# Kernel optimization log

Measured on AMD Instinct MI355X. Metric: run time of the kernel, lower is better.

## Reference

```python
import jax, jax.numpy as jnp
import numpy as np
import math

V = 32000      # vocab_size
D = 1024       # hidden_dims
T_MAX = 1024   # max_txt_len
L = 4          # n_layers
H = 8          # heads (fixed in CausalMHA)
HD = D // H
B, T = 2, 1024
EPS = 1e-5


def setup_inputs() -> dict:
    key = jax.random.key(0)
    ks = jax.random.split(key, 20)
    s = 0.02
    inp = {
        "x": jax.random.randint(ks[0], (B, T), 0, V, dtype=jnp.int64) if jax.config.read("jax_enable_x64") else jax.random.randint(ks[0], (B, T), 0, V, dtype=jnp.int32),
        "tok_emb": jax.random.normal(ks[1], (V, D), jnp.float32) * s,
        "pos_emb": jax.random.normal(ks[2], (1, T_MAX, D), jnp.float32) * s,
        "ln1_g": jnp.ones((L, D), jnp.float32),
        "ln1_b": jnp.zeros((L, D), jnp.float32),
        "wqkv": jax.random.normal(ks[3], (L, D, 3 * D), jnp.float32) * s,
        "bqkv": jnp.zeros((L, 3 * D), jnp.float32),
        "wo": jax.random.normal(ks[4], (L, D, D), jnp.float32) * s,
        "bo": jnp.zeros((L, D), jnp.float32),
        "ln2_g": jnp.ones((L, D), jnp.float32),
        "ln2_b": jnp.zeros((L, D), jnp.float32),
        "wfc": jax.random.normal(ks[5], (L, D, 4 * D), jnp.float32) * s,   # no bias
        "wfc2": jax.random.normal(ks[6], (L, 4 * D, D), jnp.float32) * s,  # no bias
        "fn_g": jnp.ones((D,), jnp.float32),
        "fn_b": jnp.zeros((D,), jnp.float32),
        "wout": jax.random.normal(ks[7], (D, V), jnp.float32) * s,
        "bout": jnp.zeros((V,), jnp.float32),
    }
    return inp


def _ln(x, g, b):
    mu = jnp.mean(x, axis=-1, keepdims=True)
    var = jnp.var(x, axis=-1, keepdims=True)
    return (x - mu) * jax.lax.rsqrt(var + EPS) * g + b


def _attn(xn, wqkv_l, bqkv_l, wo_l, bo_l):
    Bb, Tt, _ = xn.shape
    qkv = xn @ wqkv_l + bqkv_l                      # [B,T,3D]
    q, k, v = jnp.split(qkv, 3, axis=-1)
    q = q.reshape(Bb, Tt, H, HD)
    k = k.reshape(Bb, Tt, H, HD)
    v = v.reshape(Bb, Tt, H, HD)
    scores = jnp.einsum("bqhd,bkhd->bhqk", q, k) / math.sqrt(HD)
    mask = jnp.triu(jnp.ones((Tt, Tt), bool), k=1)   # True above diagonal
    scores = jnp.where(mask, jnp.float32(-jnp.inf), scores)
    att = jax.nn.softmax(scores, axis=-1)
    out = jnp.einsum("bhqk,bkhd->bqhd", att, v).reshape(Bb, Tt, D)
    return out @ wo_l + bo_l


def reference(x, tok_emb, pos_emb, ln1_g, ln1_b, wqkv, bqkv, wo, bo,
              ln2_g, ln2_b, wfc, wfc2, fn_g, fn_b, wout, bout):
    Tt = x.shape[1]
    h = tok_emb[x] + pos_emb[:, :Tt, :]              # [B,T,D]
    for i in range(L):
        h = h + _attn(_ln(h, ln1_g[i], ln1_b[i]), wqkv[i], bqkv[i], wo[i], bo[i])
        hn = _ln(h, ln2_g[i], ln2_b[i])
        h = h + jax.nn.gelu(hn @ wfc[i], approximate=False) @ wfc2[i]
    h = _ln(h, fn_g, fn_b)
    return h @ wout + bout                           # [B,T,V] logits
```

## Files before the change

### kernel.cpp

```cpp
#include <hip/hip_runtime.h>
#include <math.h>
#include <stdint.h>

#define D_  1024
#define T_  1024
#define H_  8
#define HD_ 128
#define L_  4
#define V_  32000
#define M_  2048

typedef __attribute__((ext_vector_type(4))) float f32x4;
typedef __attribute__((ext_vector_type(4))) short s16x4;
typedef __attribute__((ext_vector_type(8))) short s16x8;
typedef unsigned short u16;

__device__ __forceinline__ u16 f2bf(float f) {
  union { float f; uint32_t u; } c; c.f = f;
  uint32_t r = c.u + 0x7fffu + ((c.u >> 16) & 1u);
  return (u16)(r >> 16);
}
__device__ __forceinline__ float bf2f(u16 h) {
  union { uint32_t u; float f; } c; c.u = ((uint32_t)h) << 16;
  return c.f;
}
__device__ __forceinline__ float gelu_f(float x) {
  return 0.5f * x * (1.0f + erff(x * 0.70710678118654752f));
}

__device__ __forceinline__ void gload16(const u16* g, u16* l) {
  __builtin_amdgcn_global_load_lds(
      (const __attribute__((address_space(1))) void*)(uintptr_t)g,
      (__attribute__((address_space(3))) void*)(uint32_t)(uintptr_t)l,
      16, 0, 0);
}

__device__ __forceinline__ void convT_f32_tile(const float* __restrict__ in,
                                               u16* __restrict__ out,
                                               int ldin, int ldout,
                                               int c0, int r0,
                                               u16 (*tile)[72])
{
  const int t = threadIdx.x;
  const int rr = t >> 2, cs = (t & 3) << 4;
  u16 tmp[16];
  const float* p = in + (size_t)(r0 + rr) * ldin + c0 + cs;
#pragma unroll
  for (int q = 0; q < 4; ++q) {
    f32x4 v = *(const f32x4*)(p + q * 4);
#pragma unroll
    for (int j = 0; j < 4; ++j) tmp[q * 4 + j] = f2bf(v[j]);
  }
  *(s16x8*)&tile[rr][cs]     = *(const s16x8*)tmp;
  *(s16x8*)&tile[rr][cs + 8] = *(const s16x8*)(tmp + 8);
  __syncthreads();
  const int cr = t >> 2, rs = (t & 3) << 4;
  u16 o[16];
#pragma unroll
  for (int j = 0; j < 16; ++j) o[j] = tile[rs + j][cr];
  u16* op = out + (size_t)(c0 + cr) * ldout + r0 + rs;
  *(s16x8*)op       = *(const s16x8*)o;
  *(s16x8*)(op + 8) = *(const s16x8*)(o + 8);
}

__device__ __forceinline__
void ln_row_body(int row, float* __restrict__ hbuf, const float* __restrict__ P,
                 const float* __restrict__ g, const float* __restrict__ b,
                 u16* __restrict__ y, int red, float* red_s)
{
  const int tid = threadIdx.x;
  const size_t i = (size_t)row * D_ + tid * 4;
  f32x4 v = *(const f32x4*)&hbuf[i];
  if (red) {
#pragma unroll
    for (int zp = 0; zp < 4; ++zp) {
      f32x4 p = *(const f32x4*)&P[(size_t)zp * M_ * D_ + i];
      v[0] += p[0]; v[1] += p[1]; v[2] += p[2]; v[3] += p[3];
    }
    *(f32x4*)&hbuf[i] = v;
  }
  float s  = v[0] + v[1] + v[2] + v[3];
  float s2 = v[0]*v[0] + v[1]*v[1] + v[2]*v[2] + v[3]*v[3];
#pragma unroll
  for (int off = 32; off > 0; off >>= 1) {
    s  += __shfl_xor(s, off);
    s2 += __shfl_xor(s2, off);
  }
  if ((tid & 63) == 0) { red_s[tid >> 6] = s; red_s[4 + (tid >> 6)] = s2; }
  __syncthreads();
  s  = red_s[0] + red_s[1] + red_s[2] + red_s[3];
  s2 = red_s[4] + red_s[5] + red_s[6] + red_s[7];
  const float mean = s * (1.0f / D_);
  const float var  = s2 * (1.0f / D_) - mean * mean;
  const float rs   = rsqrtf(var + 1e-5f);
  f32x4 gg = *(const f32x4*)&g[tid * 4];
  f32x4 bb = *(const f32x4*)&b[tid * 4];
  u16 o[4];
#pragma unroll
  for (int j = 0; j < 4; ++j) o[j] = f2bf((v[j] - mean) * rs * gg[j] + bb[j]);
  *(s16x4*)&y[i] = *(const s16x4*)o;
}

__global__ __launch_bounds__(256)
void conv4ln_kernel(const float* __restrict__ wqkv_l, const float* __restrict__ wo_l,
                    const float* __restrict__ wfc_l, const float* __restrict__ wfc2_l,
                    u16* __restrict__ Wq, u16* __restrict__ Wo,
                    u16* __restrict__ Wf1, u16* __restrict__ Wf2,
                    float* __restrict__ hbuf, const float* __restrict__ P,
                    const float* __restrict__ g, const float* __restrict__ b,
                    u16* __restrict__ y, int red)
{
  __shared__ __align__(16) u16 tile[64][72];
  int f = blockIdx.x;
  if (f < 2048) { ln_row_body(f, hbuf, P, g, b, y, red, (float*)tile); return; }
  f -= 2048;
  if (f < 768) {
    convT_f32_tile(wqkv_l, Wq, 3 * D_, D_, (f % 48) << 6, (f / 48) << 6, tile);
  } else if (f < 1024) {
    f -= 768;
    convT_f32_tile(wo_l, Wo, D_, D_, (f & 15) << 6, (f >> 4) << 6, tile);
  } else if (f < 2048) {
    f -= 1024;
    convT_f32_tile(wfc_l, Wf1, 4 * D_, D_, (f & 63) << 6, (f >> 6) << 6, tile);
  } else {
    f -= 2048;
    convT_f32_tile(wfc2_l, Wf2, D_, 4 * D_, (f & 15) << 6, (f >> 4) << 6, tile);
  }
}

__global__ __launch_bounds__(256)
void convwout_ln(const float* __restrict__ wout, u16* __restrict__ WoutT,
                 float* __restrict__ hbuf, const float* __restrict__ P,
                 const float* __restrict__ g, const float* __restrict__ b,
                 u16* __restrict__ y)
{
  __shared__ __align__(16) u16 tile[64][72];
  int f = blockIdx.x;
  if (f < 2048) { ln_row_body(f, hbuf, P, g, b, y, 1, (float*)tile); return; }
  f -= 2048;
  convT_f32_tile(wout, WoutT, V_, D_, (f % 500) << 6, (f / 500) << 6, tile);
}

__global__ __launch_bounds__(256)
void ln_fold4(float* __restrict__ hbuf, const float* __restrict__ P,
              const float* __restrict__ bo, const float* __restrict__ g,
              const float* __restrict__ b, u16* __restrict__ y)
{
  __shared__ float red_s[8];
  const int row = blockIdx.x, tid = threadIdx.x;
  const size_t i = (size_t)row * D_ + tid * 4;
  f32x4 v = *(const f32x4*)&hbuf[i];
  f32x4 bb4 = *(const f32x4*)&bo[tid * 4];
#pragma unroll
  for (int zp = 0; zp < 4; ++zp) {
    f32x4 p = *(const f32x4*)&P[(size_t)zp * M_ * D_ + i];
    v[0] += p[0]; v[1] += p[1]; v[2] += p[2]; v[3] += p[3];
  }
#pragma unroll
  for (int j = 0; j < 4; ++j) v[j] += bb4[j];
  *(f32x4*)&hbuf[i] = v;
  float s  = v[0] + v[1] + v[2] + v[3];
  float s2 = v[0]*v[0] + v[1]*v[1] + v[2]*v[2] + v[3]*v[3];
#pragma unroll
  for (int off = 32; off > 0; off >>= 1) {
    s  += __shfl_xor(s, off);
    s2 += __shfl_xor(s2, off);
  }
  if ((tid & 63) == 0) { red_s[tid >> 6] = s; red_s[4 + (tid >> 6)] = s2; }
  __syncthreads();
  s  = red_s[0] + red_s[1] + red_s[2] + red_s[3];
  s2 = red_s[4] + red_s[5] + red_s[6] + red_s[7];
  const float mean = s * (1.0f / D_);
  const float var  = s2 * (1.0f / D_) - mean * mean;
  const float rs   = rsqrtf(var + 1e-5f);
  f32x4 gg = *(const f32x4*)&g[tid * 4];
  f32x4 bbn = *(const f32x4*)&b[tid * 4];
  u16 o[4];
#pragma unroll
  for (int j = 0; j < 4; ++j) o[j] = f2bf((v[j] - mean) * rs * gg[j] + bbn[j]);
  *(s16x4*)&y[i] = *(const s16x4*)o;
}

template<int OUT, int ACT, int BIAS, int VSPLIT, int KT>
__device__ __forceinline__
void gemm8n_body(const u16* __restrict__ A, int lda,
                 const u16* __restrict__ Bw, int ldb,
                 const float* __restrict__ bias,
                 void* __restrict__ Cv, int ldc, int bx, int by,
                 u16* __restrict__ VtOut)
{
  const int m0 = bx << 8, n0 = by << 7;

  __shared__ __align__(16) u16 lds[49152];

  const int tid = threadIdx.x, lane = tid & 63, wave = tid >> 6;
  const int wm = wave >> 1, wn = wave & 1;
  const int l15 = lane & 15, l4 = lane >> 4;

  f32x4 acc[4][4];
  const f32x4 z4 = {0.f, 0.f, 0.f, 0.f};
#pragma unroll
  for (int i = 0; i < 4; ++i)
#pragma unroll
    for (int j = 0; j < 4; ++j) acc[i][j] = z4;

  auto stgA = [&](int buf, int kt, int kh) {
    kt = (kt < KT - 1) ? kt : (KT - 1);
    const int slot = buf * 24576 + kh * 8192;
#pragma unroll
    for (int r = 0; r < 2; ++r) {
      const int u = r * 512 + (wave << 6) + lane;
      const int rw = u >> 2, ks = u & 3;
      const int ksw = ks ^ ((rw >> 1) & 3);
      gload16(A + (size_t)(m0 + rw) * lda + (kt << 6) + (kh << 5) + (ksw << 3),
              &lds[slot + r * 4096 + (wave << 9)]);
    }
  };
  auto stgB = [&](int buf, int kt, int kh) {
    kt = (kt < KT - 1) ? kt : (KT - 1);
    const int slot = buf * 24576 + 16384 + kh * 4096;
    const int u = (wave << 6) + lane;
    const int rw = u >> 2, ks = u & 3;
    const int ksw = ks ^ ((rw >> 1) & 3);
    gload16(Bw + (size_t)(n0 + rw) * ldb + (kt << 6) + (kh << 5) + (ksw << 3),
            &lds[slot + (wave << 9)]);
  };

  s16x8 af[4], bfr[4];

#define LDABN(bb, kk)                                                         \
  {                                                                           \
    _Pragma("unroll") for (int f = 0; f < 4; ++f) {                           \
      const int rw = wm * 64 + f * 16 + l15;                                  \
      af[f] = *(const s16x8*)&lds[(bb) + (kk) * 8192 + rw * 32 +              \
                                  ((l4 ^ ((rw >> 1) & 3)) << 3)];             \
    }                                                                         \
    _Pragma("unroll") for (int f = 0; f < 4; ++f) {                           \
      const int rn = wn * 64 + f * 16 + l15;                                  \
      bfr[f] = *(const s16x8*)&lds[(bb) + 16384 + (kk) * 4096 + rn * 32 +     \
                                   ((l4 ^ ((rn >> 1) & 3)) << 3)];            \
    }                                                                         \
  }
#define MFMAN()                                                               \
  {                                                                           \
    __builtin_amdgcn_s_barrier();                                             \
    asm volatile("s_waitcnt lgkmcnt(0)" ::: "memory");                        \
    __builtin_amdgcn_sched_barrier(0);                                        \
    __builtin_amdgcn_s_setprio(1);                                            \
    _Pragma("unroll") for (int f = 0; f < 4; ++f)                             \
      _Pragma("unroll") for (int nf = 0; nf < 4; ++nf)                        \
        acc[f][nf] = __builtin_amdgcn_mfma_f32_16x16x32_bf16(                 \
            af[f], bfr[nf], acc[f][nf], 0, 0, 0);                             \
    __builtin_amdgcn_s_setprio(0);                                            \
  }
#define BARN() __builtin_amdgcn_s_barrier()
#define VM6()  asm volatile("s_waitcnt vmcnt(6)" ::: "memory")

  stgA(0, 0, 0); stgB(0, 0, 0);
  stgA(0, 0, 1); stgB(0, 0, 1);
  stgA(1, 1, 0); stgB(1, 1, 0);
  VM6();
  BARN();

  for (int i = 0; i < KT / 2; ++i) {
    const int t = 2 * i;
    LDABN(0, 0);
    stgA(1, t + 1, 1); stgB(1, t + 1, 1);
    MFMAN(); VM6(); BARN();
    LDABN(0, 1);
    stgA(0, t + 2, 0); stgB(0, t + 2, 0);
    MFMAN(); VM6(); BARN();
    LDABN(24576, 0);
    stgA(0, t + 2, 1); stgB(0, t + 2, 1);
    MFMAN(); VM6(); BARN();
    LDABN(24576, 1);
    stgA(1, t + 3, 0); stgB(1, t + 3, 0);
    MFMAN(); VM6(); BARN();
  }
#undef LDABN
#undef MFMAN
#undef BARN
#undef VM6

  if (VSPLIT && n0 >= 2048) {
#pragma unroll
    for (int mf = 0; mf < 4; ++mf) {
      const int row0 = m0 + wm * 64 + mf * 16 + l4 * 4;
      const int bb = row0 >> 10, t0 = row0 & 1023;
#pragma unroll
      for (int nf = 0; nf < 4; ++nf) {
        const int col = n0 + wn * 64 + nf * 16 + l15;
        const float bv = BIAS ? bias[col] : 0.0f;
        u16 o4[4];
#pragma unroll
        for (int r = 0; r < 4; ++r) o4[r] = f2bf(acc[mf][nf][r] + bv);
        *(s16x4*)&VtOut[((size_t)(bb << 10) + (col - 2048)) * 1024 + t0] =
            *(const s16x4*)o4;
      }
    }
    return;
  }
  float* Cf = (float*)Cv;
  u16*   Ch = (u16*)Cv;
#pragma unroll
  for (int mf = 0; mf < 4; ++mf) {
    const int row0 = m0 + wm * 64 + mf * 16 + l4 * 4;
#pragma unroll
    for (int nf = 0; nf < 4; ++nf) {
      const int col = n0 + wn * 64 + nf * 16 + l15;
      const float bv = BIAS ? bias[col] : 0.0f;
#pragma unroll
      for (int r = 0; r < 4; ++r) {
        float v = acc[mf][nf][r] + bv;
        if (ACT) v = gelu_f(v);
        const size_t idx = (size_t)(row0 + r) * ldc + col;
        if (OUT == 0) Ch[idx] = f2bf(v);
        else          Cf[idx] = v;
      }
    }
  }
}

__global__ __launch_bounds__(512, 1)
void gemm8n_qkv(const u16* A, const u16* Bw, const float* bias, u16* C, u16* Vt) {
  int flat = blockIdx.x;
  int swz = (flat & 7) * 24 + (flat >> 3);
  gemm8n_body<0, 0, 1, 1, 16>(A, 1024, Bw, 1024, bias, C, 3 * D_,
                              swz & 7, swz >> 3, Vt);
}
__global__ __launch_bounds__(512, 1)
void gemm8n_wo(const u16* A, const u16* Bw, float* P) {
  int flat = blockIdx.x;
  int swz = (flat & 7) * 32 + (flat >> 3);
  const int bx = swz & 7, by = (swz >> 3) & 7, z = swz >> 6;
  gemm8n_body<1, 0, 0, 0, 4>(A + z * 256, 1024, Bw + z * 256, 1024, nullptr,
                             P + (size_t)z * M_ * D_, 1024, bx, by, nullptr);
}
__global__ __launch_bounds__(512, 1)
void gemm8n_fc1(const u16* A, const u16* Bw, void* Cv) {
  int flat = blockIdx.x;
  int swz = (flat & 7) * 32 + (flat >> 3);
  gemm8n_body<0, 1, 0, 0, 16>(A, 1024, Bw, 1024, nullptr, Cv, 4096,
                              swz & 7, swz >> 3, nullptr);
}
__global__ __launch_bounds__(512, 1)
void gemm8n_fc2(const u16* A, const u16* Bw, float* P) {
  int flat = blockIdx.x;
  int swz = (flat & 7) * 32 + (flat >> 3);
  const int bx = swz & 7, by = (swz >> 3) & 7, z = swz >> 6;
  gemm8n_body<1, 0, 0, 0, 16>(A + z * 1024, 4096, Bw + z * 1024, 4096, nullptr,
                              P + (size_t)z * M_ * D_, 1024, bx, by, nullptr);
}

__global__ __launch_bounds__(512, 2)
void gemm8_logits(const u16* __restrict__ A, const u16* __restrict__ Bw,
                  const float* __restrict__ bias, float* __restrict__ C)
{
  int flat = blockIdx.x;
  int swz = (flat & 7) * 125 + (flat >> 3);
  const int bx = swz & 7;
  const int by = swz >> 3;
  const int m0 = bx << 8, n0 = by << 8;

  __shared__ __align__(16) u16 lds[65536];

  const int tid = threadIdx.x, lane = tid & 63, wave = tid >> 6;
  const int wm = wave >> 2, wn = wave & 3;
  const int l15 = lane & 15, l4 = lane >> 4;

  f32x4 acc[8][4];
  const f32x4 z4 = {0.f, 0.f, 0.f, 0.f};
#pragma unroll
  for (int i = 0; i < 8; ++i)
#pragma unroll
    for (int j = 0; j < 4; ++j) acc[i][j] = z4;

  auto stg = [&](const u16* G, int rowbase, int slot, int kt, int kh) {
    kt = (kt < 15) ? kt : 15;
#pragma unroll
    for (int r = 0; r < 2; ++r) {
      const int u = r * 512 + (wave << 6) + lane;
      const int rw = u >> 2, ks = u & 3;
      const int ksw = ks ^ ((rw >> 1) & 3);
      const u16* src = G + (size_t)(rowbase + rw) * 1024 + (kt << 6) + (kh << 5) + (ksw << 3);
      gload16(src, &lds[slot + r * 4096 + (wave << 9)]);
    }
  };

  s16x8 af[4], bfr[4];

#define LDA4(bb, kk, mh)                                                      \
  {                                                                           \
    _Pragma("unroll") for (int f = 0; f < 4; ++f) {                           \
      const int rw = wm * 128 + (mh) * 64 + f * 16 + l15;                     \
      af[f] = *(const s16x8*)&lds[(bb) + (kk) * 8192 + rw * 32 +              \
                                  ((l4 ^ ((rw >> 1) & 3)) << 3)];             \
    }                                                                         \
  }
#define LDB4(bb, kk)                                                          \
  {                                                                           \
    _Pragma("unroll") for (int f = 0; f < 4; ++f) {                           \
      const int rn = wn * 64 + f * 16 + l15;                                  \
      bfr[f] = *(const s16x8*)&lds[(bb) + 16384 + (kk) * 8192 + rn * 32 +     \
                                   ((l4 ^ ((rn >> 1) & 3)) << 3)];            \
    }                                                                         \
  }
#define MFMA16(mh)                                                            \
  {                                                                           \
    __builtin_amdgcn_s_barrier();                                             \
    asm volatile("s_waitcnt lgkmcnt(0)" ::: "memory");                        \
    __builtin_amdgcn_sched_barrier(0);                                        \
    __builtin_amdgcn_s_setprio(1);                                            \
    _Pragma("unroll") for (int f = 0; f < 4; ++f)                             \
      _Pragma("unroll") for (int nf = 0; nf < 4; ++nf)                        \
        acc[(mh) * 4 + f][nf] = __builtin_amdgcn_mfma_f32_16x16x32_bf16(      \
            af[f], bfr[nf], acc[(mh) * 4 + f][nf], 0, 0, 0);                  \
    __builtin_amdgcn_s_setprio(0);                                            \
  }
#define BAR() __builtin_amdgcn_s_barrier()
#define VM4() asm volatile("s_waitcnt vmcnt(4)" ::: "memory")

  stg(A,  m0, 0,             0, 0);
  stg(Bw, n0, 16384,         0, 0);
  stg(A,  m0, 8192,          0, 1);
  stg(Bw, n0, 16384 + 8192,  0, 1);
  stg(A,  m0, 32768,         1, 0);
  stg(Bw, n0, 32768 + 16384, 1, 0);
  VM4();
  BAR();

  for (int i = 0; i < 8; ++i) {
    const int t = 2 * i;
    LDA4(0, 0, 0); LDB4(0, 0);
    stg(A, m0, 32768 + 8192, t + 1, 1);
    MFMA16(0); BAR();
    LDA4(0, 0, 1);
    stg(Bw, n0, 32768 + 24576, t + 1, 1);
    MFMA16(1); BAR();
    LDA4(0, 1, 0); LDB4(0, 1);
    stg(A, m0, 0, t + 2, 0);
    MFMA16(0); BAR();
    LDA4(0, 1, 1);
    stg(Bw, n0, 16384, t + 2, 0);
    MFMA16(1); VM4(); BAR();
    LDA4(32768, 0, 0); LDB4(32768, 0);
    stg(A, m0, 8192, t + 2, 1);
    MFMA16(0); BAR();
    LDA4(32768, 0, 1);
    stg(Bw, n0, 16384 + 8192, t + 2, 1);
    MFMA16(1); BAR();
    LDA4(32768, 1, 0); LDB4(32768, 1);
    stg(A, m0, 32768, t + 3, 0);
    MFMA16(0); BAR();
    LDA4(32768, 1, 1);
    stg(Bw, n0, 32768 + 16384, t + 3, 0);
    MFMA16(1); VM4(); BAR();
  }
#undef LDA4
#undef LDB4
#undef MFMA16
#undef BAR
#undef VM4

  float bv[4];
#pragma unroll
  for (int nf = 0; nf < 4; ++nf) bv[nf] = bias[n0 + wn * 64 + nf * 16 + l15];
#pragma unroll
  for (int mf = 0; mf < 8; ++mf) {
    const int row0 = m0 + wm * 128 + mf * 16 + l4 * 4;
#pragma unroll
    for (int nf = 0; nf < 4; ++nf) {
      const int col = n0 + wn * 64 + nf * 16 + l15;
#pragma unroll
      for (int r = 0; r < 4; ++r)
        C[(size_t)(row0 + r) * V_ + col] = acc[mf][nf][r] + bv[nf];
    }
  }
}

__global__ __launch_bounds__(128)
void flash_attn(const u16* __restrict__ qkv, const u16* __restrict__ Vt,
                u16* __restrict__ xo)
{
  int flat = blockIdx.x;
  int swz = (flat & 7) * 64 + (flat >> 3);
  const int qb = 31 - (swz & 31);
  const int z  = swz >> 5;
  const int b  = z >> 3, hh = z & 7;

  __shared__ __align__(16) u16 Ks[64 * 128];
  __shared__ __align__(16) u16 Vs[128 * 64];
  __shared__ __align__(16) u16 Ps[32 * 80];

  const int tid = threadIdx.x, lane = tid & 63, w = tid >> 6;
  const int l15 = lane & 15, l4 = lane >> 4;
  const float iscale = 0.08838834764831845f;

  const int qrow = qb * 32 + w * 16 + l15;
  const u16* qptr = qkv + ((size_t)(b * T_) + qrow) * (3 * D_) + hh * HD_;

  s16x8 bQ[4];
#pragma unroll
  for (int ks = 0; ks < 4; ++ks)
    bQ[ks] = *(const s16x8*)(qptr + ks * 32 + l4 * 8);

  f32x4 O[8];
#pragma unroll
  for (int i = 0; i < 8; ++i) O[i] = {0.f, 0.f, 0.f, 0.f};
  float m_run = -1e30f, l_run = 0.f;

  const int ntiles = (qb >> 1) + 1;
  for (int kt = 0; kt < ntiles; ++kt) {
    __syncthreads();
    {
      const int r = tid >> 1, c0 = (tid & 1) << 6;
      const u16* src = qkv + ((size_t)(b * T_) + kt * 64 + r) * (3 * D_) + D_ + hh * HD_ + c0;
#pragma unroll
      for (int u = 0; u < 8; ++u) {
        s16x8 v = *(const s16x8*)(src + u * 8);
        const int dblk = (c0 >> 3) + u;
        *(s16x8*)&Ks[r * 128 + ((dblk ^ (r & 7)) << 3)] = v;
      }
      const int d = tid;
      const u16* vsrc = Vt + ((size_t)z * HD_ + d) * T_ + kt * 64;
#pragma unroll
      for (int u = 0; u < 8; ++u) {
        s16x8 v = *(const s16x8*)(vsrc + u * 8);
        *(s16x8*)&Vs[d * 64 + ((u ^ (d & 7)) << 3)] = v;
      }
    }
    __syncthreads();

    f32x4 st[4];
#pragma unroll
    for (int mf = 0; mf < 4; ++mf) st[mf] = {0.f, 0.f, 0.f, 0.f};
#pragma unroll
    for (int ks = 0; ks < 4; ++ks) {
      s16x8 aK[4];
#pragma unroll
      for (int mf = 0; mf < 4; ++mf) {
        const int r = mf * 16 + l15;
        aK[mf] = *(const s16x8*)&Ks[r * 128 + ((((ks << 2) + l4) ^ (r & 7)) << 3)];
      }
#pragma unroll
      for (int mf = 0; mf < 4; ++mf)
        st[mf] = __builtin_amdgcn_mfma_f32_16x16x32_bf16(aK[mf], bQ[ks], st[mf], 0, 0, 0);
    }

    const bool diag = (kt == ntiles - 1);
    float sv[16];
    float mx = -1e30f;
#pragma unroll
    for (int mf = 0; mf < 4; ++mf)
#pragma unroll
      for (int r = 0; r < 4; ++r) {
        float s = st[mf][r] * iscale;
        if (diag) {
          const int k = kt * 64 + mf * 16 + l4 * 4 + r;
          if (k > qrow) s = -1e30f;
        }
        sv[mf * 4 + r] = s;
        mx = fmaxf(mx, s);
      }
    mx = fmaxf(mx, __shfl_xor(mx, 16));
    mx = fmaxf(mx, __shfl_xor(mx, 32));
    const float m_new = fmaxf(m_run, mx);
    const float sc_old = __expf(m_run - m_new);
    float psum = 0.f;
    u16 pb[16];
#pragma unroll
    for (int j = 0; j < 16; ++j) {
      const float p = __expf(sv[j] - m_new);
      psum += p;
      pb[j] = f2bf(p);
    }
    psum += __shfl_xor(psum, 16);
    psum += __shfl_xor(psum, 32);
    l_run = l_run * sc_old + psum;
    m_run = m_new;

    float scr[4];
#pragma unroll
    for (int r = 0; r < 4; ++r) scr[r] = __shfl(sc_old, l4 * 4 + r);
#pragma unroll
    for (int df = 0; df < 8; ++df)
#pragma unroll
      for (int r = 0; r < 4; ++r) O[df][r] *= scr[r];

    {
      const int row = w * 16 + l15;
#pragma unroll
      for (int j = 0; j < 16; ++j) {
        const int k = (j >> 2) * 16 + l4 * 4 + (j & 3);
        Ps[row * 80 + (((k >> 3) ^ (l15 & 7)) << 3) + (k & 7)] = pb[j];
      }
    }

#pragma unroll
    for (int kc = 0; kc < 2; ++kc) {
      const int prow = w * 16 + l15;
      s16x8 aP = *(const s16x8*)&Ps[prow * 80 + ((((kc << 2) + l4) ^ (l15 & 7)) << 3)];
#pragma unroll
      for (int df = 0; df < 8; ++df) {
        const int d = df * 16 + l15;
        s16x8 bV = *(const s16x8*)&Vs[d * 64 + ((((kc << 2) + l4) ^ (d & 7)) << 3)];
        O[df] = __builtin_amdgcn_mfma_f32_16x16x32_bf16(aP, bV, O[df], 0, 0, 0);
      }
    }
  }

  const float inv_l = 1.0f / l_run;
  float invr[4];
#pragma unroll
  for (int r = 0; r < 4; ++r) invr[r] = __shfl(inv_l, l4 * 4 + r);
#pragma unroll
  for (int df = 0; df < 8; ++df)
#pragma unroll
    for (int r = 0; r < 4; ++r) {
      const int row = qb * 32 + w * 16 + l4 * 4 + r;
      xo[((size_t)(b * T_) + row) * D_ + hh * HD_ + df * 16 + l15] =
          f2bf(O[df][r] * invr[r]);
    }
}

__global__ __launch_bounds__(256)
void embed_kernel(const int* __restrict__ x, const float* __restrict__ tok,
                  const float* __restrict__ pos, float* __restrict__ h)
{
  const int row = blockIdx.x, tid = threadIdx.x;
  const int t = row & (T_ - 1);
  const int id = x[row];
  f32x4 a = *(const f32x4*)&tok[(size_t)id * D_ + tid * 4];
  f32x4 p = *(const f32x4*)&pos[(size_t)t * D_ + tid * 4];
  f32x4 o = {a[0] + p[0], a[1] + p[1], a[2] + p[2], a[3] + p[3]};
  *(f32x4*)&h[(size_t)row * D_ + tid * 4] = o;
}

extern "C" void kernel_launch(void* const* d_in, const int* in_sizes, int n_in,
                              void* d_out, int out_size, void* d_ws, size_t ws_size,
                              hipStream_t stream)
{
  (void)in_sizes; (void)n_in; (void)out_size; (void)ws_size;
  const int*   x     = (const int*)  d_in[0];
  const float* tok   = (const float*)d_in[1];
  const float* pos   = (const float*)d_in[2];
  const float* ln1_g = (const float*)d_in[3];
  const float* ln1_b = (const float*)d_in[4];
  const float* wqkv  = (const float*)d_in[5];
  const float* bqkv  = (const float*)d_in[6];
  const float* wo    = (const float*)d_in[7];
  const float* bo    = (const float*)d_in[8];
  const float* ln2_g = (const float*)d_in[9];
  const float* ln2_b = (const float*)d_in[10];
  const float* wfc   = (const float*)d_in[11];
  const float* wfc2  = (const float*)d_in[12];
  const float* fn_g  = (const float*)d_in[13];
  const float* fn_b  = (const float*)d_in[14];
  const float* wout  = (const float*)d_in[15];
  const float* bout  = (const float*)d_in[16];
  float* out = (float*)d_out;

  float* h  = (float*)d_ws;
  u16* xn   = (u16*)(h + (size_t)M_ * D_);
  u16* Wq   = xn  + (size_t)M_ * D_;
  u16* Wo   = Wq  + (size_t)3 * D_ * D_;
  u16* Wf1  = Wo  + (size_t)D_ * D_;
  u16* Wf2  = Wf1 + (size_t)4 * D_ * D_;
  u16* qkv  = Wf2 + (size_t)4 * D_ * D_;
  u16* Vt   = qkv + (size_t)M_ * 3 * D_;
  u16* S    = Vt  + (size_t)2 * T_ * D_;
  float* P  = (float*)(S + (size_t)M_ * 4 * D_);
  u16* WoutT = Wq;

  embed_kernel<<<M_, 256, 0, stream>>>(x, tok, pos, h);

  for (int l = 0; l < L_; ++l) {
    conv4ln_kernel<<<5120, 256, 0, stream>>>(
        wqkv + (size_t)l * D_ * 3 * D_, wo + (size_t)l * D_ * D_,
        wfc + (size_t)l * D_ * 4 * D_, wfc2 + (size_t)l * 4 * D_ * D_,
        Wq, Wo, Wf1, Wf2,
        h, P, ln1_g + l * D_, ln1_b + l * D_, xn, l > 0 ? 1 : 0);
    gemm8n_qkv<<<192, 512, 0, stream>>>(xn, Wq, bqkv + l * 3 * D_, qkv, Vt);
    flash_attn<<<512, 128, 0, stream>>>(qkv, Vt, xn);
    gemm8n_wo<<<256, 512, 0, stream>>>(xn, Wo, P);
    ln_fold4<<<M_, 256, 0, stream>>>(h, P, bo + l * D_,
                                     ln2_g + l * D_, ln2_b + l * D_, xn);
    gemm8n_fc1<<<256, 512, 0, stream>>>(xn, Wf1, S);
    gemm8n_fc2<<<256, 512, 0, stream>>>(S, Wf2, P);
  }

  convwout_ln<<<10048, 256, 0, stream>>>(wout, WoutT, h, P, fn_g, fn_b, xn);
  gemm8_logits<<<1000, 512, 0, stream>>>(xn, WoutT, bout, out);
}
```

Baseline: 841.8 us.

## Rewrite logits GEMM with 256x128 tiles and 3-stage LDS pipeline

The logits GEMM moves from 512-thread blocks with 256x256 tiles and a two-buffer, half-K staged schedule to 256-thread blocks with 256x128 tiles. Each block walks K in 32-wide steps through a 3-deep ring of LDS buffers, with one barrier per step. Smaller LDS use and smaller blocks aim for better occupancy and simpler overlap of loads with MFMA. In exchange, the grid doubles to 2000 blocks, the A tile is re-read more often, and the loop now runs more iterations with a synchronization point at each one.

```diff
diff --git a/kernel.cpp b/kernel.cpp
--- a/kernel.cpp
+++ b/kernel.cpp
@@ -352,20 +352,20 @@
                               P + (size_t)z * M_ * D_, 1024, bx, by, nullptr);
 }
 
-__global__ __launch_bounds__(512, 2)
-void gemm8_logits(const u16* __restrict__ A, const u16* __restrict__ Bw,
-                  const float* __restrict__ bias, float* __restrict__ C)
+__global__ __launch_bounds__(256, 2)
+void gemm3b_logits(const u16* __restrict__ A, const u16* __restrict__ Bw,
+                   const float* __restrict__ bias, float* __restrict__ C)
 {
   int flat = blockIdx.x;
-  int swz = (flat & 7) * 125 + (flat >> 3);
+  int swz = (flat & 7) * 250 + (flat >> 3);
   const int bx = swz & 7;
   const int by = swz >> 3;
-  const int m0 = bx << 8, n0 = by << 8;
-
-  __shared__ __align__(16) u16 lds[65536];
+  const int m0 = bx << 8, n0 = by << 7;
+
+  __shared__ __align__(16) u16 lds[36864];
 
   const int tid = threadIdx.x, lane = tid & 63, wave = tid >> 6;
-  const int wm = wave >> 2, wn = wave & 3;
+  const int wm = wave >> 1, wn = wave & 1;
   const int l15 = lane & 15, l4 = lane >> 4;
 
   f32x4 acc[8][4];
@@ -375,92 +375,80 @@
 #pragma unroll
     for (int j = 0; j < 4; ++j) acc[i][j] = z4;
 
-  auto stg = [&](const u16* G, int rowbase, int slot, int kt, int kh) {
-    kt = (kt < 15) ? kt : 15;
-#pragma unroll
-    for (int r = 0; r < 2; ++r) {
-      const int u = r * 512 + (wave << 6) + lane;
+  auto stgA = [&](int buf, int kt) {
+    kt = (kt < 31) ? kt : 31;
+    const int slot = buf * 12288;
+#pragma unroll
+    for (int r = 0; r < 4; ++r) {
+      const int u = r * 256 + (wave << 6) + lane;
       const int rw = u >> 2, ks = u & 3;
       const int ksw = ks ^ ((rw >> 1) & 3);
-      const u16* src = G + (size_t)(rowbase + rw) * 1024 + (kt << 6) + (kh << 5) + (ksw << 3);
-      gload16(src, &lds[slot + r * 4096 + (wave << 9)]);
+      gload16(A + (size_t)(m0 + rw) * 1024 + (kt << 5) + (ksw << 3),
+              &lds[slot + r * 2048 + (wave << 9)]);
     }
   };
-
-  s16x8 af[4], bfr[4];
-
-#define LDA4(bb, kk, mh)                                                      \
+  auto stgB = [&](int buf, int kt) {
+    kt = (kt < 31) ? kt : 31;
+    const int slot = buf * 12288 + 8192;
+#pragma unroll
+    for (int r = 0; r < 2; ++r) {
+      const int u = r * 256 + (wave << 6) + lane;
+      const int rw = u >> 2, ks = u & 3;
+      const int ksw = ks ^ ((rw >> 1) & 3);
+      gload16(Bw + (size_t)(n0 + rw) * 1024 + (kt << 5) + (ksw << 3),
+              &lds[slot + r * 2048 + (wave << 9)]);
+    }
+  };
+
+  s16x8 af[8], bfr[4];
+
+#define LDAB3(bb)                                                             \
   {                                                                           \
-    _Pragma("unroll") for (int f = 0; f < 4; ++f) {                           \
-      const int rw = wm * 128 + (mh) * 64 + f * 16 + l15;                     \
-      af[f] = *(const s16x8*)&lds[(bb) + (kk) * 8192 + rw * 32 +              \
+    _Pragma("unroll") for (int f = 0; f < 8; ++f) {                           \
+      const int rw = wm * 128 + f * 16 + l15;                                 \
+      af[f] = *(const s16x8*)&lds[(bb) + rw * 32 +                            \
                                   ((l4 ^ ((rw >> 1) & 3)) << 3)];             \
     }                                                                         \
-  }
-#define LDB4(bb, kk)                                                          \
-  {                                                                           \
     _Pragma("unroll") for (int f = 0; f < 4; ++f) {                           \
       const int rn = wn * 64 + f * 16 + l15;                                  \
-      bfr[f] = *(const s16x8*)&lds[(bb) + 16384 + (kk) * 8192 + rn * 32 +     \
+      bfr[f] = *(const s16x8*)&lds[(bb) + 8192 + rn * 32 +                    \
                                    ((l4 ^ ((rn >> 1) & 3)) << 3)];            \
     }                                                                         \
   }
-#define MFMA16(mh)                                                            \
+#define MFMA3()                                                               \
   {                                                                           \
     __builtin_amdgcn_s_barrier();                                             \
     asm volatile("s_waitcnt lgkmcnt(0)" ::: "memory");                        \
     __builtin_amdgcn_sched_barrier(0);                                        \
     __builtin_amdgcn_s_setprio(1);                                            \
-    _Pragma("unroll") for (int f = 0; f < 4; ++f)                             \
+    _Pragma("unroll") for (int f = 0; f < 8; ++f)                             \
       _Pragma("unroll") for (int nf = 0; nf < 4; ++nf)                        \
-        acc[(mh) * 4 + f][nf] = __builtin_amdgcn_mfma_f32_16x16x32_bf16(      \
-            af[f], bfr[nf], acc[(mh) * 4 + f][nf], 0, 0, 0);                  \
+        acc[f][nf] = __builtin_amdgcn_mfma_f32_16x16x32_bf16(                 \
+            af[f], bfr[nf], acc[f][nf], 0, 0, 0);                             \
     __builtin_amdgcn_s_setprio(0);                                            \
   }
-#define BAR() __builtin_amdgcn_s_barrier()
-#define VM4() asm volatile("s_waitcnt vmcnt(4)" ::: "memory")
-
-  stg(A,  m0, 0,             0, 0);
-  stg(Bw, n0, 16384,         0, 0);
-  stg(A,  m0, 8192,          0, 1);
-  stg(Bw, n0, 16384 + 8192,  0, 1);
-  stg(A,  m0, 32768,         1, 0);
-  stg(Bw, n0, 32768 + 16384, 1, 0);
-  VM4();
-  BAR();
-
-  for (int i = 0; i < 8; ++i) {
-    const int t = 2 * i;
-    LDA4(0, 0, 0); LDB4(0, 0);
-    stg(A, m0, 32768 + 8192, t + 1, 1);
-    MFMA16(0); BAR();
-    LDA4(0, 0, 1);
-    stg(Bw, n0, 32768 + 24576, t + 1, 1);
-    MFMA16(1); BAR();
-    LDA4(0, 1, 0); LDB4(0, 1);
-    stg(A, m0, 0, t + 2, 0);
-    MFMA16(0); BAR();
-    LDA4(0, 1, 1);
-    stg(Bw, n0, 16384, t + 2, 0);
-    MFMA16(1); VM4(); BAR();
-    LDA4(32768, 0, 0); LDB4(32768, 0);
-    stg(A, m0, 8192, t + 2, 1);
-    MFMA16(0); BAR();
-    LDA4(32768, 0, 1);
-    stg(Bw, n0, 16384 + 8192, t + 2, 1);
-    MFMA16(1); BAR();
-    LDA4(32768, 1, 0); LDB4(32768, 1);
-    stg(A, m0, 32768, t + 3, 0);
-    MFMA16(0); BAR();
-    LDA4(32768, 1, 1);
-    stg(Bw, n0, 32768 + 16384, t + 3, 0);
-    MFMA16(1); VM4(); BAR();
-  }
-#undef LDA4
-#undef LDB4
-#undef MFMA16
-#undef BAR
-#undef VM4
+#define BAR3() __builtin_amdgcn_s_barrier()
+#define VM6L() asm volatile("s_waitcnt vmcnt(6)" ::: "memory")
+
+  stgA(0, 0); stgB(0, 0);
+  stgA(1, 1); stgB(1, 1);
+  VM6L();
+  BAR3();
+
+#pragma unroll 1
+  for (int t = 0; t < 32; ++t) {
+    const int buf  = t - (t / 3) * 3;
+    const int nbuf = (t + 2) - ((t + 2) / 3) * 3;
+    LDAB3(buf * 12288);
+    stgA(nbuf, t + 2); stgB(nbuf, t + 2);
+    MFMA3();
+    VM6L();
+    BAR3();
+  }
+#undef LDAB3
+#undef MFMA3
+#undef BAR3
+#undef VM6L
 
   float bv[4];
 #pragma unroll
@@ -690,5 +678,5 @@
   }
 
   convwout_ln<<<10048, 256, 0, stream>>>(wout, WoutT, h, P, fn_g, fn_b, xn);
-  gemm8_logits<<<1000, 512, 0, stream>>>(xn, WoutT, bout, out);
-}
+  gemm3b_logits<<<2000, 256, 0, stream>>>(xn, WoutT, bout, out);
+}
```

Measured after the change: 841.7 us. No clear change (-0.0%).
